# Kernel tuning notes

Hardware: AMD Instinct MI355X
Metric: run time of the kernel (lower is better)

Reference implementation:

```python
import jax, jax.numpy as jnp
import numpy as np

N_NODES = 10000
N_EDGES = 160000
D_IN = 512
D_HID = 1024

def setup_inputs() -> dict:
    key = jax.random.key(0)
    ks = jax.random.split(key, 8)
    feat = jax.random.normal(ks[0], (N_NODES, D_IN), dtype=jnp.float32)
    W1 = jax.random.normal(ks[1], (D_IN, D_HID), dtype=jnp.float32) * (1.0 / np.sqrt(D_IN))
    b1 = jnp.zeros((D_HID,), dtype=jnp.float32)
    W2 = jax.random.normal(ks[2], (D_HID, D_IN), dtype=jnp.float32) * (1.0 / np.sqrt(D_HID))
    b2 = jnp.zeros((D_IN,), dtype=jnp.float32)
    eps = jnp.zeros((1,), dtype=jnp.float32)
    src = jax.random.randint(ks[3], (N_EDGES,), 0, N_NODES, dtype=jnp.int32)
    dst = jax.random.randint(ks[4], (N_EDGES,), 0, N_NODES, dtype=jnp.int32)
    return {"feat": feat, "W1": W1, "b1": b1, "W2": W2, "b2": b2,
            "eps": eps, "src": src, "dst": dst}

def reference(feat, W1, b1, W2, b2, eps, src, dst):
    # message passing: copy src feature along each edge, sum-reduce at dst
    msgs = feat[src]                                   # [E, D_IN] gather
    neigh = jax.ops.segment_sum(msgs, dst, num_segments=feat.shape[0])  # [N, D_IN]
    # GIN combine: (1 + eps) * self + sum(neighbors)
    rst = (1.0 + eps[0]) * feat + neigh
    # apply_func: 2-layer MLP with ReLU
    h = jnp.maximum(rst @ W1 + b1, 0.0)
    h = h @ W2 + b2
    # identity residual (in_dim == out_dim)
    return h + feat
```

## Files before the change

### kernel.cpp

```cpp
#include <hip/hip_runtime.h>

typedef unsigned short u16;
typedef unsigned int u32;
typedef __bf16 bf16x8 __attribute__((ext_vector_type(8)));
typedef float f32x4 __attribute__((ext_vector_type(4)));

#define N_NODES 10000
#define N_EDGES 160000
#define D_IN 512
#define D_HID 1024

#define AS1 __attribute__((address_space(1)))
#define AS3 __attribute__((address_space(3)))

__device__ __forceinline__ u16 f2bf(float f) {
    union { float f; u32 u; } v; v.f = f;
    return (u16)((v.u + 0x7fffu + ((v.u >> 16) & 1u)) >> 16);
}
__device__ __forceinline__ float b2f(u32 h) {
    union { u32 u; float f; } v; v.u = h << 16; return v.f;
}

__global__ void hist_k(const int* __restrict__ dst, int* __restrict__ counts) {
    int e = blockIdx.x * 256 + threadIdx.x;
    if (e < N_EDGES) atomicAdd(&counts[dst[e]], 1);
}

__global__ __launch_bounds__(1024) void scan_k(const int* __restrict__ counts,
                                               int* __restrict__ offs,
                                               int* __restrict__ cursor) {
    __shared__ int wpre[16];
    int t = threadIdx.x, l = t & 63, w = t >> 6;
    int base = t * 10;
    int c[10];
    int lsum = 0;
#pragma unroll
    for (int i = 0; i < 10; i++) {
        int idx = base + i;
        c[i] = (idx < N_NODES) ? counts[idx] : 0;
        lsum += c[i];
    }
    int sc = lsum;
#pragma unroll
    for (int d = 1; d < 64; d <<= 1) {
        int v = __shfl_up(sc, d);
        if (l >= d) sc += v;
    }
    __shared__ int wsum[16];
    if (l == 63) wsum[w] = sc;
    __syncthreads();
    if (w == 0 && l < 16) {
        int v = wsum[l];
        int p = v;
#pragma unroll
        for (int d = 1; d < 16; d <<= 1) {
            int u = __shfl_up(p, d);
            if (l >= d) p += u;
        }
        wpre[l] = p - v;
    }
    __syncthreads();
    int run = wpre[w] + sc - lsum;
#pragma unroll
    for (int i = 0; i < 10; i++) {
        int idx = base + i;
        if (idx < N_NODES) { offs[idx] = run; cursor[idx] = run; run += c[i]; }
    }
    if (t == 1023) offs[N_NODES] = wpre[15] + sc;
}

__global__ void reorder_k(const int* __restrict__ src, const int* __restrict__ dst,
                          int* __restrict__ cursor, int* __restrict__ ssrc) {
    int e = blockIdx.x * 256 + threadIdx.x;
    if (e >= N_EDGES) return;
    int d = dst[e];
    int pos = atomicAdd(&cursor[d], 1);
    ssrc[pos] = src[e];
}

__global__ void cvt_bf16_k(const float* __restrict__ in, u16* __restrict__ out, int n) {
    int i = (blockIdx.x * 256 + threadIdx.x) * 8;
    if (i >= n) return;
    float4 a = *(const float4*)(in + i);
    float4 b = *(const float4*)(in + i + 4);
    uint4 o;
    o.x = (u32)f2bf(a.x) | ((u32)f2bf(a.y) << 16);
    o.y = (u32)f2bf(a.z) | ((u32)f2bf(a.w) << 16);
    o.z = (u32)f2bf(b.x) | ((u32)f2bf(b.y) << 16);
    o.w = (u32)f2bf(b.z) | ((u32)f2bf(b.w) << 16);
    *(uint4*)(out + i) = o;
}

__global__ void transw_k(const float* __restrict__ W1, u16* __restrict__ w1t,
                         const float* __restrict__ W2, u16* __restrict__ w2t) {
    __shared__ float tile[32][33];
    int b = blockIdx.x;
    const float* W; u16* WT; int K, N, nt;
    if (b < 512) { W = W1; WT = w1t; K = D_IN;  N = D_HID; nt = 32; }
    else         { b -= 512; W = W2; WT = w2t; K = D_HID; N = D_IN;  nt = 16; }
    int n0 = (b % nt) * 32, k0 = (b / nt) * 32;
    int tx = threadIdx.x, ty = threadIdx.y;
#pragma unroll
    for (int i = 0; i < 32; i += 8)
        tile[ty + i][tx] = W[(size_t)(k0 + ty + i) * N + n0 + tx];
    __syncthreads();
#pragma unroll
    for (int i = 0; i < 32; i += 8)
        WT[(size_t)(n0 + ty + i) * K + k0 + tx] = f2bf(tile[tx][ty + i]);
}

__global__ __launch_bounds__(128) void gather_k(const float* __restrict__ feat,
                                                const u16* __restrict__ featb,
                                                const float* __restrict__ eps,
                                                const int* __restrict__ offs,
                                                const int* __restrict__ ssrc,
                                                u16* __restrict__ out) {
    int n = (blockIdx.x * 128 + threadIdx.x) >> 6;
    int l = threadIdx.x & 63;
    if (n >= N_NODES) return;
    int beg = offs[n], end = offs[n + 1];
    float s = 1.0f + eps[0];
    float4 s0 = *(const float4*)(feat + (size_t)n * D_IN + l * 8);
    float4 s1 = *(const float4*)(feat + (size_t)n * D_IN + l * 8 + 4);
    float acc[8] = { s * s0.x, s * s0.y, s * s0.z, s * s0.w,
                     s * s1.x, s * s1.y, s * s1.z, s * s1.w };
    int e = beg;
    for (; e + 4 <= end; e += 4) {
        int i0 = ssrc[e], i1 = ssrc[e + 1], i2 = ssrc[e + 2], i3 = ssrc[e + 3];
        uint4 v0 = *(const uint4*)(featb + (size_t)i0 * D_IN + l * 8);
        uint4 v1 = *(const uint4*)(featb + (size_t)i1 * D_IN + l * 8);
        uint4 v2 = *(const uint4*)(featb + (size_t)i2 * D_IN + l * 8);
        uint4 v3 = *(const uint4*)(featb + (size_t)i3 * D_IN + l * 8);
#define ACC4(v) \
        acc[0] += b2f(v.x & 0xffffu); acc[1] += b2f(v.x >> 16); \
        acc[2] += b2f(v.y & 0xffffu); acc[3] += b2f(v.y >> 16); \
        acc[4] += b2f(v.z & 0xffffu); acc[5] += b2f(v.z >> 16); \
        acc[6] += b2f(v.w & 0xffffu); acc[7] += b2f(v.w >> 16);
        ACC4(v0) ACC4(v1) ACC4(v2) ACC4(v3)
    }
    for (; e < end; e++) {
        int i0 = ssrc[e];
        uint4 v0 = *(const uint4*)(featb + (size_t)i0 * D_IN + l * 8);
        ACC4(v0)
    }
#undef ACC4
    uint4 o;
    o.x = (u32)f2bf(acc[0]) | ((u32)f2bf(acc[1]) << 16);
    o.y = (u32)f2bf(acc[2]) | ((u32)f2bf(acc[3]) << 16);
    o.z = (u32)f2bf(acc[4]) | ((u32)f2bf(acc[5]) << 16);
    o.w = (u32)f2bf(acc[6]) | ((u32)f2bf(acc[7]) << 16);
    *(uint4*)(out + (size_t)n * D_IN + l * 8) = o;
}

template <int EPI>
__global__ __launch_bounds__(256) void gemm_k(const u16* __restrict__ A,
                                              const u16* __restrict__ BT,
                                              const float* __restrict__ bias,
                                              const float* __restrict__ feat,
                                              void* __restrict__ Cout,
                                              int M, int N, int K) {
    __shared__ __bf16 sA[128 * 64];
    __shared__ __bf16 sB[128 * 64];
    const int row0 = blockIdx.y * 128;
    const int col0 = blockIdx.x * 128;
    const int t = threadIdx.x;
    const int w = t >> 6, l = t & 63;
    const int wm = (w >> 1) * 64, wn = (w & 1) * 64;
    const int lr = l & 15;
    const int lq = l >> 4;

    const u16* pA[4];
    const u16* pB[4];
    __bf16* lA[4];
    __bf16* lB[4];
    {
        int rloc = w * 32 + (l >> 3);
        int gch8 = (((l & 7) ^ (l >> 3)) * 8);
#pragma unroll
        for (int q = 0; q < 4; q++) {
            int ar = row0 + rloc + q * 8; if (ar > M - 1) ar = M - 1;
            pA[q] = A + (size_t)ar * K + gch8;
            int br = col0 + rloc + q * 8;
            pB[q] = BT + (size_t)br * K + gch8;
            lA[q] = sA + (w * 32 + q * 8) * 64;
            lB[q] = sB + (w * 32 + q * 8) * 64;
        }
    }
    const int fo = ((lq ^ (lr & 7)) * 8);

    f32x4 acc[4][4] = {};

    for (int k0 = 0; k0 < K; k0 += 64) {
        __syncthreads();
#pragma unroll
        for (int q = 0; q < 4; q++) {
            __builtin_amdgcn_global_load_lds((const AS1 void*)(pA[q] + k0),
                                             (AS3 void*)lA[q], 16, 0, 0);
            __builtin_amdgcn_global_load_lds((const AS1 void*)(pB[q] + k0),
                                             (AS3 void*)lB[q], 16, 0, 0);
        }
        __syncthreads();
#pragma unroll
        for (int kk = 0; kk < 64; kk += 32) {
            const int fx = fo ^ kk;
            bf16x8 fa[4], fb[4];
#pragma unroll
            for (int i = 0; i < 4; i++)
                fa[i] = *(const bf16x8*)(sA + (wm + i * 16 + lr) * 64 + fx);
#pragma unroll
            for (int j = 0; j < 4; j++)
                fb[j] = *(const bf16x8*)(sB + (wn + j * 16 + lr) * 64 + fx);
#pragma unroll
            for (int i = 0; i < 4; i++)
#pragma unroll
                for (int j = 0; j < 4; j++)
                    acc[i][j] = __builtin_amdgcn_mfma_f32_16x16x32_bf16(
                        fa[i], fb[j], acc[i][j], 0, 0, 0);
        }
    }

#pragma unroll
    for (int i = 0; i < 4; i++) {
        int rowb = row0 + wm + i * 16 + lq * 4;
#pragma unroll
        for (int j = 0; j < 4; j++) {
            int col = col0 + wn + j * 16 + lr;
            float bv = bias[col];
#pragma unroll
            for (int r = 0; r < 4; r++) {
                int rr = rowb + r;
                if (rr < M) {
                    float v = acc[i][j][r] + bv;
                    if (EPI == 0) {
                        v = fmaxf(v, 0.0f);
                        ((u16*)Cout)[(size_t)rr * N + col] = f2bf(v);
                    } else {
                        v += feat[(size_t)rr * N + col];
                        ((float*)Cout)[(size_t)rr * N + col] = v;
                    }
                }
            }
        }
    }
}

extern "C" void kernel_launch(void* const* d_in, const int* in_sizes, int n_in,
                              void* d_out, int out_size, void* d_ws, size_t ws_size,
                              hipStream_t stream) {
    const float* feat = (const float*)d_in[0];
    const float* W1   = (const float*)d_in[1];
    const float* b1   = (const float*)d_in[2];
    const float* W2   = (const float*)d_in[3];
    const float* b2   = (const float*)d_in[4];
    const float* eps  = (const float*)d_in[5];
    const int*   src  = (const int*)d_in[6];
    const int*   dst  = (const int*)d_in[7];
    float* out = (float*)d_out;

    char* ws = (char*)d_ws;
    u16* rst_b16 = (u16*)(ws);
    u16* h_b16   = (u16*)(ws + 10240000);
    u16* featb   = (u16*)(ws + 30720000);
    u16* w1t     = (u16*)(ws + 40960000);
    u16* w2t     = (u16*)(ws + 42008576);
    int* counts  = (int*)(ws + 43057152);
    int* offs    = (int*)(ws + 43097152);
    int* cursor  = (int*)(ws + 43137160);
    int* ssrc    = (int*)(ws + 43177160);

    const int NE = N_NODES * D_IN;

    hipMemsetAsync(counts, 0, N_NODES * sizeof(int), stream);
    hist_k<<<(N_EDGES + 255) / 256, 256, 0, stream>>>(dst, counts);
    scan_k<<<1, 1024, 0, stream>>>(counts, offs, cursor);
    reorder_k<<<(N_EDGES + 255) / 256, 256, 0, stream>>>(src, dst, cursor, ssrc);

    cvt_bf16_k<<<NE / 8 / 256, 256, 0, stream>>>(feat, featb, NE);
    transw_k<<<1024, dim3(32, 8), 0, stream>>>(W1, w1t, W2, w2t);

    gather_k<<<(N_NODES + 1) / 2, 128, 0, stream>>>(feat, featb, eps, offs, ssrc, rst_b16);

    const int MT = (N_NODES + 127) / 128;
    gemm_k<0><<<dim3(D_HID / 128, MT), 256, 0, stream>>>(rst_b16, w1t, b1, nullptr,
                                                         (void*)h_b16, N_NODES, D_HID, D_IN);
    gemm_k<1><<<dim3(D_IN / 128, MT), 256, 0, stream>>>(h_b16, w2t, b2, feat,
                                                        (void*)out, N_NODES, D_IN, D_HID);
}
```

Baseline: 206.9 us.

## Double-buffer GEMM LDS tiles with K-step 32 to overlap loads and MFMA

Replaces the single 64-wide K tile in shared memory with two 32-wide buffers. The next tile's global-to-LDS loads are issued before the current tile's MFMAs, leaving one barrier per iteration instead of two. The LDS swizzle is redone for the 32-element row layout. The aim is to hide global load latency behind compute. The cost is twice as many loop iterations, each doing half the MFMA work per barrier.

```diff
diff --git a/kernel.cpp b/kernel.cpp
--- a/kernel.cpp
+++ b/kernel.cpp
@@ -159,8 +159,8 @@
                                               const float* __restrict__ feat,
                                               void* __restrict__ Cout,
                                               int M, int N, int K) {
-    __shared__ __bf16 sA[128 * 64];
-    __shared__ __bf16 sB[128 * 64];
+    __shared__ __bf16 sA[2][128 * 32];
+    __shared__ __bf16 sB[2][128 * 32];
     const int row0 = blockIdx.y * 128;
     const int col0 = blockIdx.x * 128;
     const int t = threadIdx.x;
@@ -169,54 +169,62 @@
     const int lr = l & 15;
     const int lq = l >> 4;
 
-    const u16* pA[4];
-    const u16* pB[4];
-    __bf16* lA[4];
-    __bf16* lB[4];
+    const u16* pA[2];
+    const u16* pB[2];
+    int ldsoff[2];
     {
-        int rloc = w * 32 + (l >> 3);
-        int gch8 = (((l & 7) ^ (l >> 3)) * 8);
-#pragma unroll
-        for (int q = 0; q < 4; q++) {
-            int ar = row0 + rloc + q * 8; if (ar > M - 1) ar = M - 1;
-            pA[q] = A + (size_t)ar * K + gch8;
-            int br = col0 + rloc + q * 8;
-            pB[q] = BT + (size_t)br * K + gch8;
-            lA[q] = sA + (w * 32 + q * 8) * 64;
-            lB[q] = sB + (w * 32 + q * 8) * 64;
-        }
-    }
-    const int fo = ((lq ^ (lr & 7)) * 8);
+        int rloc = w * 32 + (l >> 2);
+        int gch = (((l & 3) ^ ((l >> 3) & 3)) * 8);
+#pragma unroll
+        for (int q = 0; q < 2; q++) {
+            int ar = row0 + rloc + q * 16; if (ar > M - 1) ar = M - 1;
+            pA[q] = A + (size_t)ar * K + gch;
+            int br = col0 + rloc + q * 16;
+            pB[q] = BT + (size_t)br * K + gch;
+            ldsoff[q] = (w * 32 + q * 16) * 32;
+        }
+    }
+    const int fo = ((lq ^ ((lr >> 1) & 3)) * 8);
 
     f32x4 acc[4][4] = {};
-
-    for (int k0 = 0; k0 < K; k0 += 64) {
+    const int NI = K >> 5;
+
+#pragma unroll
+    for (int q = 0; q < 2; q++) {
+        __builtin_amdgcn_global_load_lds((const AS1 void*)pA[q],
+                                         (AS3 void*)(&sA[0][ldsoff[q]]), 16, 0, 0);
+        __builtin_amdgcn_global_load_lds((const AS1 void*)pB[q],
+                                         (AS3 void*)(&sB[0][ldsoff[q]]), 16, 0, 0);
+    }
+    __syncthreads();
+
+    for (int k = 0; k < NI; k++) {
+        int kn = k + 1;
+        if (kn < NI) {
+            int kb = kn & 1, ko = kn << 5;
+#pragma unroll
+            for (int q = 0; q < 2; q++) {
+                __builtin_amdgcn_global_load_lds((const AS1 void*)(pA[q] + ko),
+                                                 (AS3 void*)(&sA[kb][ldsoff[q]]), 16, 0, 0);
+                __builtin_amdgcn_global_load_lds((const AS1 void*)(pB[q] + ko),
+                                                 (AS3 void*)(&sB[kb][ldsoff[q]]), 16, 0, 0);
+            }
+        }
+        const int cb = k & 1;
+        bf16x8 fa[4], fb[4];
+#pragma unroll
+        for (int i = 0; i < 4; i++)
+            fa[i] = *(const bf16x8*)(&sA[cb][(wm + i * 16 + lr) * 32 + fo]);
+#pragma unroll
+        for (int j = 0; j < 4; j++)
+            fb[j] = *(const bf16x8*)(&sB[cb][(wn + j * 16 + lr) * 32 + fo]);
+#pragma unroll
+        for (int i = 0; i < 4; i++)
+#pragma unroll
+            for (int j = 0; j < 4; j++)
+                acc[i][j] = __builtin_amdgcn_mfma_f32_16x16x32_bf16(
+                    fa[i], fb[j], acc[i][j], 0, 0, 0);
         __syncthreads();
-#pragma unroll
-        for (int q = 0; q < 4; q++) {
-            __builtin_amdgcn_global_load_lds((const AS1 void*)(pA[q] + k0),
-                                             (AS3 void*)lA[q], 16, 0, 0);
-            __builtin_amdgcn_global_load_lds((const AS1 void*)(pB[q] + k0),
-                                             (AS3 void*)lB[q], 16, 0, 0);
-        }
-        __syncthreads();
-#pragma unroll
-        for (int kk = 0; kk < 64; kk += 32) {
-            const int fx = fo ^ kk;
-            bf16x8 fa[4], fb[4];
-#pragma unroll
-            for (int i = 0; i < 4; i++)
-                fa[i] = *(const bf16x8*)(sA + (wm + i * 16 + lr) * 64 + fx);
-#pragma unroll
-            for (int j = 0; j < 4; j++)
-                fb[j] = *(const bf16x8*)(sB + (wn + j * 16 + lr) * 64 + fx);
-#pragma unroll
-            for (int i = 0; i < 4; i++)
-#pragma unroll
-                for (int j = 0; j < 4; j++)
-                    acc[i][j] = __builtin_amdgcn_mfma_f32_16x16x32_bf16(
-                        fa[i], fb[j], acc[i][j], 0, 0, 0);
-        }
     }
 
 #pragma unroll
```

Result: slower. 213.8 us (+3.3%).

## Restructure GEMM to stage full-K B panel in LDS and stream A from global

Applied to the files above, without the earlier changes.

The GEMM kernel now holds a 64-column by 512-deep slice of the transposed weight in padded LDS and reads A fragments directly from global memory into registers. A and B fragments are prefetched with a rotating register pipeline, so the per-64-K double barrier loop goes away. The column tile halves, which doubles the number of blocks and the re-reads of A. A loads are now uncoalesced per lane from global, and the larger LDS footprint may lower occupancy.

```diff
diff --git a/kernel.cpp b/kernel.cpp
--- a/kernel.cpp
+++ b/kernel.cpp
@@ -152,6 +152,9 @@
     *(uint4*)(out + (size_t)n * D_IN + l * 8) = o;
 }
 
+#define BCOL 64
+#define KC 512
+#define LDB 520
 template <int EPI>
 __global__ __launch_bounds__(256) void gemm_k(const u16* __restrict__ A,
                                               const u16* __restrict__ BT,
@@ -159,63 +162,65 @@
                                               const float* __restrict__ feat,
                                               void* __restrict__ Cout,
                                               int M, int N, int K) {
-    __shared__ __bf16 sA[128 * 64];
-    __shared__ __bf16 sB[128 * 64];
+    __shared__ __bf16 sB[BCOL * LDB];
     const int row0 = blockIdx.y * 128;
-    const int col0 = blockIdx.x * 128;
+    const int col0 = blockIdx.x * BCOL;
     const int t = threadIdx.x;
     const int w = t >> 6, l = t & 63;
-    const int wm = (w >> 1) * 64, wn = (w & 1) * 64;
+    const int wm = (w >> 1) * 64;
+    const int wn = (w & 1) * 32;
     const int lr = l & 15;
     const int lq = l >> 4;
 
-    const u16* pA[4];
-    const u16* pB[4];
-    __bf16* lA[4];
-    __bf16* lB[4];
-    {
-        int rloc = w * 32 + (l >> 3);
-        int gch8 = (((l & 7) ^ (l >> 3)) * 8);
-#pragma unroll
-        for (int q = 0; q < 4; q++) {
-            int ar = row0 + rloc + q * 8; if (ar > M - 1) ar = M - 1;
-            pA[q] = A + (size_t)ar * K + gch8;
-            int br = col0 + rloc + q * 8;
-            pB[q] = BT + (size_t)br * K + gch8;
-            lA[q] = sA + (w * 32 + q * 8) * 64;
-            lB[q] = sB + (w * 32 + q * 8) * 64;
-        }
-    }
-    const int fo = ((lq ^ (lr & 7)) * 8);
-
-    f32x4 acc[4][4] = {};
-
-    for (int k0 = 0; k0 < K; k0 += 64) {
+    const u16* pa[4];
+#pragma unroll
+    for (int i = 0; i < 4; i++) {
+        int r = row0 + wm + i * 16 + lr; if (r > M - 1) r = M - 1;
+        pa[i] = A + (size_t)r * K + lq * 8;
+    }
+
+    f32x4 acc[4][2] = {};
+
+    for (int kc = 0; kc < K; kc += KC) {
+        if (kc) __syncthreads();
+#pragma unroll
+        for (int ci = 0; ci < 16; ci++) {
+            int c = w * 16 + ci;
+            __builtin_amdgcn_global_load_lds(
+                (const AS1 void*)(BT + (size_t)(col0 + c) * K + kc + l * 8),
+                (AS3 void*)(sB + c * LDB), 16, 0, 0);
+        }
         __syncthreads();
-#pragma unroll
-        for (int q = 0; q < 4; q++) {
-            __builtin_amdgcn_global_load_lds((const AS1 void*)(pA[q] + k0),
-                                             (AS3 void*)lA[q], 16, 0, 0);
-            __builtin_amdgcn_global_load_lds((const AS1 void*)(pB[q] + k0),
-                                             (AS3 void*)lB[q], 16, 0, 0);
-        }
-        __syncthreads();
-#pragma unroll
-        for (int kk = 0; kk < 64; kk += 32) {
-            const int fx = fo ^ kk;
-            bf16x8 fa[4], fb[4];
+
+        bf16x8 fa[3][4];
+        bf16x8 fbb[2][2];
+#pragma unroll
+        for (int i = 0; i < 4; i++) fa[0][i] = *(const bf16x8*)(pa[i] + kc);
+#pragma unroll
+        for (int i = 0; i < 4; i++) fa[1][i] = *(const bf16x8*)(pa[i] + kc + 32);
+#pragma unroll
+        for (int j = 0; j < 2; j++)
+            fbb[0][j] = *(const bf16x8*)(sB + (wn + j * 16 + lr) * LDB + lq * 8);
+
+#pragma unroll
+        for (int s = 0; s < 16; s++) {
+            if (s + 2 < 16) {
+#pragma unroll
+                for (int i = 0; i < 4; i++)
+                    fa[(s + 2) % 3][i] = *(const bf16x8*)(pa[i] + kc + (s + 2) * 32);
+            }
+            if (s + 1 < 16) {
+#pragma unroll
+                for (int j = 0; j < 2; j++)
+                    fbb[(s + 1) & 1][j] = *(const bf16x8*)(sB + (wn + j * 16 + lr) * LDB
+                                                           + (s + 1) * 32 + lq * 8);
+            }
 #pragma unroll
             for (int i = 0; i < 4; i++)
-                fa[i] = *(const bf16x8*)(sA + (wm + i * 16 + lr) * 64 + fx);
-#pragma unroll
-            for (int j = 0; j < 4; j++)
-                fb[j] = *(const bf16x8*)(sB + (wn + j * 16 + lr) * 64 + fx);
-#pragma unroll
-            for (int i = 0; i < 4; i++)
-#pragma unroll
-                for (int j = 0; j < 4; j++)
+#pragma unroll
+                for (int j = 0; j < 2; j++)
                     acc[i][j] = __builtin_amdgcn_mfma_f32_16x16x32_bf16(
-                        fa[i], fb[j], acc[i][j], 0, 0, 0);
+                        fa[s % 3][i], fbb[s & 1][j], acc[i][j], 0, 0, 0);
         }
     }
 
@@ -223,7 +228,7 @@
     for (int i = 0; i < 4; i++) {
         int rowb = row0 + wm + i * 16 + lq * 4;
 #pragma unroll
-        for (int j = 0; j < 4; j++) {
+        for (int j = 0; j < 2; j++) {
             int col = col0 + wn + j * 16 + lr;
             float bv = bias[col];
 #pragma unroll
@@ -281,8 +286,8 @@
     gather_k<<<(N_NODES + 1) / 2, 128, 0, stream>>>(feat, featb, eps, offs, ssrc, rst_b16);
 
     const int MT = (N_NODES + 127) / 128;
-    gemm_k<0><<<dim3(D_HID / 128, MT), 256, 0, stream>>>(rst_b16, w1t, b1, nullptr,
-                                                         (void*)h_b16, N_NODES, D_HID, D_IN);
-    gemm_k<1><<<dim3(D_IN / 128, MT), 256, 0, stream>>>(h_b16, w2t, b2, feat,
-                                                        (void*)out, N_NODES, D_IN, D_HID);
-}
+    gemm_k<0><<<dim3(D_HID / BCOL, MT), 256, 0, stream>>>(rst_b16, w1t, b1, nullptr,
+                                                          (void*)h_b16, N_NODES, D_HID, D_IN);
+    gemm_k<1><<<dim3(D_IN / BCOL, MT), 256, 0, stream>>>(h_b16, w2t, b2, feat,
+                                                         (void*)out, N_NODES, D_IN, D_HID);
+}
```

Result: slower. 274.0 us (+32.4%).

## Prefetch next GEMM K-tile into registers while computing current tile

Applied to the files above, without the earlier changes.

Replaces the direct global-to-LDS loads in the GEMM main loop with register-staged loads. The next 64-wide K slice is fetched into registers before the MFMA work on the current slice, then written to LDS after a barrier. This aims to hide global memory latency behind compute. In exchange it uses more VGPRs for staging, which may lower occupancy, and adds explicit LDS store instructions plus a change to the LDS swizzle pattern.

```diff
diff --git a/kernel.cpp b/kernel.cpp
--- a/kernel.cpp
+++ b/kernel.cpp
@@ -9,9 +9,6 @@
 #define N_EDGES 160000
 #define D_IN 512
 #define D_HID 1024
-
-#define AS1 __attribute__((address_space(1)))
-#define AS3 __attribute__((address_space(3)))
 
 __device__ __forceinline__ u16 f2bf(float f) {
     union { float f; u32 u; } v; v.f = f;
@@ -169,53 +166,68 @@
     const int lr = l & 15;
     const int lq = l >> 4;
 
-    const u16* pA[4];
-    const u16* pB[4];
-    __bf16* lA[4];
-    __bf16* lB[4];
-    {
-        int rloc = w * 32 + (l >> 3);
-        int gch8 = (((l & 7) ^ (l >> 3)) * 8);
-#pragma unroll
-        for (int q = 0; q < 4; q++) {
-            int ar = row0 + rloc + q * 8; if (ar > M - 1) ar = M - 1;
-            pA[q] = A + (size_t)ar * K + gch8;
-            int br = col0 + rloc + q * 8;
-            pB[q] = BT + (size_t)br * K + gch8;
-            lA[q] = sA + (w * 32 + q * 8) * 64;
-            lB[q] = sB + (w * 32 + q * 8) * 64;
-        }
-    }
-    const int fo = ((lq ^ (lr & 7)) * 8);
+    const int sr = t >> 3;
+    const int ss = t & 7;
+    const int sw = ss ^ (sr & 7);
+    const u16* ga[4];
+    const u16* gb[4];
+    int lo[4];
+#pragma unroll
+    for (int c = 0; c < 4; c++) {
+        int m = c * 32 + sr;
+        int ar = row0 + m; if (ar > M - 1) ar = M - 1;
+        ga[c] = A + (size_t)ar * K + ss * 8;
+        gb[c] = BT + (size_t)(col0 + m) * K + ss * 8;
+        lo[c] = m * 64 + sw * 8;
+    }
+    const int fsw = lr & 7;
 
     f32x4 acc[4][4] = {};
-
-    for (int k0 = 0; k0 < K; k0 += 64) {
-        __syncthreads();
-#pragma unroll
-        for (int q = 0; q < 4; q++) {
-            __builtin_amdgcn_global_load_lds((const AS1 void*)(pA[q] + k0),
-                                             (AS3 void*)lA[q], 16, 0, 0);
-            __builtin_amdgcn_global_load_lds((const AS1 void*)(pB[q] + k0),
-                                             (AS3 void*)lB[q], 16, 0, 0);
-        }
-        __syncthreads();
+    const int NI = K >> 6;
+
+    uint4 ra[4], rb[4];
+#pragma unroll
+    for (int c = 0; c < 4; c++) { ra[c] = *(const uint4*)ga[c]; rb[c] = *(const uint4*)gb[c]; }
+#pragma unroll
+    for (int c = 0; c < 4; c++) { *(uint4*)(&sA[lo[c]]) = ra[c]; *(uint4*)(&sB[lo[c]]) = rb[c]; }
+    __syncthreads();
+
+    for (int k = 0; k < NI; k++) {
+        if (k + 1 < NI) {
+            int ko = (k + 1) << 6;
+#pragma unroll
+            for (int c = 0; c < 4; c++) {
+                ra[c] = *(const uint4*)(ga[c] + ko);
+                rb[c] = *(const uint4*)(gb[c] + ko);
+            }
+        }
 #pragma unroll
         for (int kk = 0; kk < 64; kk += 32) {
-            const int fx = fo ^ kk;
+            const int qb = kk >> 3;
             bf16x8 fa[4], fb[4];
 #pragma unroll
             for (int i = 0; i < 4; i++)
-                fa[i] = *(const bf16x8*)(sA + (wm + i * 16 + lr) * 64 + fx);
+                fa[i] = *(const bf16x8*)(&sA[(wm + i * 16 + lr) * 64
+                                             + (((lq + qb) ^ fsw) * 8)]);
 #pragma unroll
             for (int j = 0; j < 4; j++)
-                fb[j] = *(const bf16x8*)(sB + (wn + j * 16 + lr) * 64 + fx);
+                fb[j] = *(const bf16x8*)(&sB[(wn + j * 16 + lr) * 64
+                                             + (((lq + qb) ^ fsw) * 8)]);
 #pragma unroll
             for (int i = 0; i < 4; i++)
 #pragma unroll
                 for (int j = 0; j < 4; j++)
                     acc[i][j] = __builtin_amdgcn_mfma_f32_16x16x32_bf16(
                         fa[i], fb[j], acc[i][j], 0, 0, 0);
+        }
+        __syncthreads();
+        if (k + 1 < NI) {
+#pragma unroll
+            for (int c = 0; c < 4; c++) {
+                *(uint4*)(&sA[lo[c]]) = ra[c];
+                *(uint4*)(&sB[lo[c]]) = rb[c];
+            }
+            __syncthreads();
         }
     }
 
```

After: 296.9 us. 1.43x slower.
